# Kernel optimization log

Measured on AMD Instinct MI355X. Metric: run time of the kernel, lower is better.

The kernel has to match this reference:

```python
import jax, jax.numpy as jnp
import numpy as np

INPUT_SIZE = 512
UNITS = 1024


def setup_inputs() -> dict:
    key = jax.random.key(0)
    k_x, k_wih, k_whh, k_bih, k_bhh = jax.random.split(key, 5)
    B, T = 128, 512
    s_ih = 1.0 / np.sqrt(UNITS)
    return {
        "inputs": jax.random.normal(k_x, (B, T, INPUT_SIZE), dtype=jnp.float32),
        # torch nn.LSTMCell params: gate order i, f, g, o
        "W_ih": jax.random.uniform(k_wih, (4 * UNITS, INPUT_SIZE), minval=-s_ih, maxval=s_ih, dtype=jnp.float32),
        "W_hh": jax.random.uniform(k_whh, (4 * UNITS, UNITS), minval=-s_ih, maxval=s_ih, dtype=jnp.float32),
        "b_ih": jax.random.uniform(k_bih, (4 * UNITS,), minval=-s_ih, maxval=s_ih, dtype=jnp.float32),
        "b_hh": jax.random.uniform(k_bhh, (4 * UNITS,), minval=-s_ih, maxval=s_ih, dtype=jnp.float32),
    }


def reference(inputs, W_ih, W_hh, b_ih, b_hh):
    B, T, _ = inputs.shape
    U = W_hh.shape[1]
    # Precompute input contribution for all timesteps: [B, T, 4U]
    x_gates = jnp.einsum('bti,gi->btg', inputs, W_ih) + b_ih + b_hh

    def step(carry, xg):
        h, c = carry
        gates = xg + h @ W_hh.T  # [B, 4U]
        i, f, g, o = jnp.split(gates, 4, axis=-1)
        i = jax.nn.sigmoid(i)
        f = jax.nn.sigmoid(f)
        g = jnp.tanh(g)
        o = jax.nn.sigmoid(o)
        c = f * c + i * g
        h = o * jnp.tanh(c)
        return (h, c), h

    h0 = jnp.zeros((B, U), dtype=inputs.dtype)
    c0 = jnp.zeros((B, U), dtype=inputs.dtype)
    _, hs = jax.lax.scan(step, (h0, c0), jnp.swapaxes(x_gates, 0, 1))
    return jnp.swapaxes(hs, 0, 1)  # [B, T, U] (return_sequences=True)
```

## Files before the change

kernel.cpp:

```cpp
#include <hip/hip_runtime.h>
#include <hip/hip_bf16.h>

typedef __attribute__((ext_vector_type(8))) short short8;
typedef __attribute__((ext_vector_type(4))) float f32x4;
typedef unsigned int u32;
typedef unsigned short u16;

#define T_STEPS 512
#define B_SZ    128
#define I_SZ    512
#define U_SZ    1024
#define K_TOT   1536

#define XB_OFF   0
#define WC_OFF   67108864
#define FLAG_OFF 79691776
#define HBUF_OFF 79708160

__device__ __forceinline__ u16 f2bf(float f) {
  u32 u = __float_as_uint(f);
  u32 r = (u + 0x7fffu + ((u >> 16) & 1u)) >> 16;
  return (u16)r;
}
__device__ __forceinline__ float sigm(float x) { return 1.f / (1.f + __expf(-x)); }
__device__ __forceinline__ float tanh_s(float x) {
  float ax = fabsf(x);
  float e  = __expf(-2.f * ax);
  float t  = (1.f - e) / (1.f + e);
  return copysignf(t, x);
}

__global__ void k_convX(const float* __restrict__ X, u16* __restrict__ Xb) {
  u32 i = blockIdx.x * 256u + threadIdx.x;
  float4 v = reinterpret_cast<const float4*>(X)[i];
  uint2 o;
  o.x = (u32)f2bf(v.x) | ((u32)f2bf(v.y) << 16);
  o.y = (u32)f2bf(v.z) | ((u32)f2bf(v.w) << 16);
  reinterpret_cast<uint2*>(Xb)[i] = o;
}

__global__ void k_packW(const float* __restrict__ Wih, const float* __restrict__ Whh,
                        u16* __restrict__ Wc) {
  const int gcol = blockIdx.x;
  for (int k = threadIdx.x; k < K_TOT; k += 256) {
    float v = (k < I_SZ) ? Wih[(size_t)gcol * I_SZ + k]
                         : Whh[(size_t)gcol * U_SZ + (k - I_SZ)];
    Wc[(size_t)gcol * K_TOT + k] = f2bf(v);
  }
}

__global__ void k_zero(u32* __restrict__ hz, u32* __restrict__ flags) {
  u32 i = blockIdx.x * 256u + threadIdx.x;
  if (i < 131072u)      hz[i] = 0u;
  else if (i < 131328u) flags[i - 131072u] = 0u;
}

__device__ __forceinline__ short8 ld_h16(const u16* p) {
  short8 r;
  asm volatile("global_load_dwordx4 %0, %1, off sc0 sc1" : "=v"(r) : "v"(p));
  return r;
}
__device__ __forceinline__ void st_h(u16* p, u32 v) {
  asm volatile("global_store_short %0, %1, off sc0 sc1" :: "v"(p), "v"(v) : "memory");
}
__device__ __forceinline__ short8 ld_w16(const u16* p) {
  short8 r;
  asm volatile("global_load_dwordx4 %0, %1, off" : "=v"(r) : "v"(p));
  return r;
}

__global__ __launch_bounds__(512, 2)
void lstm_scan(const u16* __restrict__ Xb, const u16* __restrict__ Wc,
               const float* __restrict__ bih, const float* __restrict__ bhh,
               u16* __restrict__ hbuf, u32* __restrict__ flags,
               float* __restrict__ out) {
  __shared__ __align__(16) float gbuf[8][64][36];

  const int tid  = threadIdx.x;
  const int wg   = blockIdx.x;
  const int cl   = wg >> 6;
  const int wloc = wg & 63;
  const int rb   = cl * 32;
  const int u0   = wloc * 16;
  const int wid  = tid >> 6;
  const int lane = tid & 63;
  const int l15  = lane & 15;
  const int kg   = lane >> 4;
  const int kw   = wid;

  short8 Bf[6][4];
  #pragma unroll
  for (int ct = 0; ct < 4; ++ct) {
    const int gcol = ct * 1024 + u0 + l15;
    const u16* wrow = Wc + (size_t)gcol * K_TOT;
    #pragma unroll
    for (int i = 0; i < 6; ++i) {
      const int k = (i * 8 + kw) * 32 + kg * 8;
      Bf[i][ct] = ld_w16(wrow + k);
    }
  }
  asm volatile("s_waitcnt vmcnt(0)" ::: "memory");
  __builtin_amdgcn_sched_barrier(0);

  const int b_l = tid >> 4;
  const int uu  = tid & 15;
  const int ug  = u0 + uu;
  float bsum[4];
  #pragma unroll
  for (int g = 0; g < 4; ++g) bsum[g] = bih[g * 1024 + ug] + bhh[g * 1024 + ug];
  float c_state = 0.f;
  float* orow = out + (size_t)(rb + b_l) * (T_STEPS * U_SZ) + ug;
  const int hidx = (rb + b_l) * U_SZ + ug;
  u32* myflag = flags + (cl << 6) + wloc;
  u32* pollp  = flags + (cl << 6) + lane;

  const int r0 = rb + l15;
  const int r1 = r0 + 16;
  const u16* xrow0 = Xb + (size_t)r0 * (T_STEPS * I_SZ);
  const u16* xrow1 = Xb + (size_t)r1 * (T_STEPS * I_SZ);

  for (int t = 0; t < T_STEPS; ++t) {
    const u16* hsrc = hbuf + ((t & 1) ^ 1) * (B_SZ * U_SZ);
    u16*       hdst = hbuf + (t & 1) * (B_SZ * U_SZ);
    const u16* px0 = xrow0 + (size_t)t * I_SZ;
    const u16* px1 = xrow1 + (size_t)t * I_SZ;

    f32x4 acc[2][4];
    #pragma unroll
    for (int rt = 0; rt < 2; ++rt)
      #pragma unroll
      for (int ct = 0; ct < 4; ++ct)
        acc[rt][ct] = (f32x4){0.f, 0.f, 0.f, 0.f};

    #pragma unroll
    for (int i = 0; i < 2; ++i) {
      const int k = (i * 8 + kw) * 32 + kg * 8;
      const short8 a0 = *reinterpret_cast<const short8*>(px0 + k);
      const short8 a1 = *reinterpret_cast<const short8*>(px1 + k);
      #pragma unroll
      for (int ct = 0; ct < 4; ++ct) {
        acc[0][ct] = __builtin_amdgcn_mfma_f32_16x16x32_bf16(a0, Bf[i][ct], acc[0][ct], 0, 0, 0);
        acc[1][ct] = __builtin_amdgcn_mfma_f32_16x16x32_bf16(a1, Bf[i][ct], acc[1][ct], 0, 0, 0);
      }
    }

    for (;;) {
      const u32 v = __hip_atomic_load(pollp, __ATOMIC_RELAXED, __HIP_MEMORY_SCOPE_AGENT);
      if (__all((int)(v >= (u32)t))) break;
      __builtin_amdgcn_s_sleep(1);
    }

    short8 hA[4][2];
    #pragma unroll
    for (int ih = 0; ih < 4; ++ih) {
      const int ku = ((2 + ih) * 8 + kw) * 32 + kg * 8 - 512;
      hA[ih][0] = ld_h16(hsrc + (size_t)r0 * U_SZ + ku);
      hA[ih][1] = ld_h16(hsrc + (size_t)r1 * U_SZ + ku);
    }
    asm volatile("s_waitcnt vmcnt(0)" ::: "memory");
    __builtin_amdgcn_sched_barrier(0);
    #pragma unroll
    for (int ih = 0; ih < 4; ++ih)
      #pragma unroll
      for (int ct = 0; ct < 4; ++ct) {
        acc[0][ct] = __builtin_amdgcn_mfma_f32_16x16x32_bf16(hA[ih][0], Bf[2 + ih][ct], acc[0][ct], 0, 0, 0);
        acc[1][ct] = __builtin_amdgcn_mfma_f32_16x16x32_bf16(hA[ih][1], Bf[2 + ih][ct], acc[1][ct], 0, 0, 0);
      }

    #pragma unroll
    for (int rt = 0; rt < 2; ++rt)
      #pragma unroll
      for (int ct = 0; ct < 4; ++ct)
        *reinterpret_cast<float4*>(&gbuf[kw][ct * 16 + l15][rt * 16 + kg * 4]) =
            *reinterpret_cast<float4*>(&acc[rt][ct]);
    __syncthreads();

    float gs[4];
    #pragma unroll
    for (int g = 0; g < 4; ++g) {
      float s = bsum[g];
      #pragma unroll
      for (int k2 = 0; k2 < 8; ++k2) s += gbuf[k2][g * 16 + uu][b_l];
      gs[g] = s;
    }
    const float ig = sigm(gs[0]);
    const float fg = sigm(gs[1]);
    const float gg = tanh_s(gs[2]);
    const float og = sigm(gs[3]);
    c_state = fg * c_state + ig * gg;
    const float h = og * tanh_s(c_state);

    st_h(hdst + hidx, (u32)f2bf(h));
    asm volatile("s_waitcnt vmcnt(0)" ::: "memory");
    __syncthreads();
    if (tid == 0)
      __hip_atomic_store(myflag, (u32)(t + 1), __ATOMIC_RELAXED, __HIP_MEMORY_SCOPE_AGENT);

    orow[(size_t)t * U_SZ] = h;
  }
}

extern "C" void kernel_launch(void* const* d_in, const int* in_sizes, int n_in,
                              void* d_out, int out_size, void* d_ws, size_t ws_size,
                              hipStream_t stream) {
  const float* X   = (const float*)d_in[0];
  const float* Wih = (const float*)d_in[1];
  const float* Whh = (const float*)d_in[2];
  const float* bih = (const float*)d_in[3];
  const float* bhh = (const float*)d_in[4];
  float* out = (float*)d_out;
  char*  ws  = (char*)d_ws;

  u16* Xb    = (u16*)(ws + XB_OFF);
  u16* Wc    = (u16*)(ws + WC_OFF);
  u32* flags = (u32*)(ws + FLAG_OFF);
  u16* hbuf  = (u16*)(ws + HBUF_OFF);

  hipLaunchKernelGGL(k_convX, dim3(32768), dim3(256), 0, stream, X, Xb);
  hipLaunchKernelGGL(k_packW, dim3(4096), dim3(256), 0, stream, Wih, Whh, Wc);
  hipLaunchKernelGGL(k_zero,  dim3(513),  dim3(256), 0, stream, (u32*)hbuf, flags);

  void* args[] = {(void*)&Xb, (void*)&Wc, (void*)&bih, (void*)&bhh,
                  (void*)&hbuf, (void*)&flags, (void*)&out};
  hipLaunchCooperativeKernel((void*)lstm_scan, dim3(256), dim3(512), args, 0, stream);
}
```

Baseline: 2.584 ms.

## Prefetch next-step input projection before barrier and poll only needed producer flags

The x-part of the gate MFMA for step t+1 is now computed right after the h store, before the store-completion wait and barrier. The goal is to hide that input projection and its global loads under the store latency and the inter-workgroup synchronization instead of leaving them on the critical path. Each wave now also polls only the flags of the workgroups whose h columns it reads, not all 64 in the cluster, which relaxes the dependency wait. The cost is the accumulators staying live across the loop boundary, which may raise register pressure.

```diff
diff --git a/kernel.cpp b/kernel.cpp
--- a/kernel.cpp
+++ b/kernel.cpp
@@ -112,37 +112,37 @@
   float* orow = out + (size_t)(rb + b_l) * (T_STEPS * U_SZ) + ug;
   const int hidx = (rb + b_l) * U_SZ + ug;
   u32* myflag = flags + (cl << 6) + wloc;
-  u32* pollp  = flags + (cl << 6) + lane;
+
+  const int pidx = (kw << 1) + (((lane >> 1) & 3) << 4) + (lane & 1);
+  const u32* pollp = flags + (cl << 6) + pidx;
 
   const int r0 = rb + l15;
   const int r1 = r0 + 16;
   const u16* xrow0 = Xb + (size_t)r0 * (T_STEPS * I_SZ);
   const u16* xrow1 = Xb + (size_t)r1 * (T_STEPS * I_SZ);
 
+  f32x4 acc[2][4];
+  #pragma unroll
+  for (int rt = 0; rt < 2; ++rt)
+    #pragma unroll
+    for (int ct = 0; ct < 4; ++ct)
+      acc[rt][ct] = (f32x4){0.f, 0.f, 0.f, 0.f};
+
+  #pragma unroll
+  for (int i = 0; i < 2; ++i) {
+    const int k = (i * 8 + kw) * 32 + kg * 8;
+    const short8 a0 = *reinterpret_cast<const short8*>(xrow0 + k);
+    const short8 a1 = *reinterpret_cast<const short8*>(xrow1 + k);
+    #pragma unroll
+    for (int ct = 0; ct < 4; ++ct) {
+      acc[0][ct] = __builtin_amdgcn_mfma_f32_16x16x32_bf16(a0, Bf[i][ct], acc[0][ct], 0, 0, 0);
+      acc[1][ct] = __builtin_amdgcn_mfma_f32_16x16x32_bf16(a1, Bf[i][ct], acc[1][ct], 0, 0, 0);
+    }
+  }
+
   for (int t = 0; t < T_STEPS; ++t) {
     const u16* hsrc = hbuf + ((t & 1) ^ 1) * (B_SZ * U_SZ);
     u16*       hdst = hbuf + (t & 1) * (B_SZ * U_SZ);
-    const u16* px0 = xrow0 + (size_t)t * I_SZ;
-    const u16* px1 = xrow1 + (size_t)t * I_SZ;
-
-    f32x4 acc[2][4];
-    #pragma unroll
-    for (int rt = 0; rt < 2; ++rt)
-      #pragma unroll
-      for (int ct = 0; ct < 4; ++ct)
-        acc[rt][ct] = (f32x4){0.f, 0.f, 0.f, 0.f};
-
-    #pragma unroll
-    for (int i = 0; i < 2; ++i) {
-      const int k = (i * 8 + kw) * 32 + kg * 8;
-      const short8 a0 = *reinterpret_cast<const short8*>(px0 + k);
-      const short8 a1 = *reinterpret_cast<const short8*>(px1 + k);
-      #pragma unroll
-      for (int ct = 0; ct < 4; ++ct) {
-        acc[0][ct] = __builtin_amdgcn_mfma_f32_16x16x32_bf16(a0, Bf[i][ct], acc[0][ct], 0, 0, 0);
-        acc[1][ct] = __builtin_amdgcn_mfma_f32_16x16x32_bf16(a1, Bf[i][ct], acc[1][ct], 0, 0, 0);
-      }
-    }
 
     for (;;) {
       const u32 v = __hip_atomic_load(pollp, __ATOMIC_RELAXED, __HIP_MEMORY_SCOPE_AGENT);
@@ -191,6 +191,29 @@
     const float h = og * tanh_s(c_state);
 
     st_h(hdst + hidx, (u32)f2bf(h));
+
+    #pragma unroll
+    for (int rt = 0; rt < 2; ++rt)
+      #pragma unroll
+      for (int ct = 0; ct < 4; ++ct)
+        acc[rt][ct] = (f32x4){0.f, 0.f, 0.f, 0.f};
+    if (t + 1 < T_STEPS) {
+      const u16* qx0 = xrow0 + (size_t)(t + 1) * I_SZ;
+      const u16* qx1 = xrow1 + (size_t)(t + 1) * I_SZ;
+      #pragma unroll
+      for (int i = 0; i < 2; ++i) {
+        const int k = (i * 8 + kw) * 32 + kg * 8;
+        const short8 a0 = *reinterpret_cast<const short8*>(qx0 + k);
+        const short8 a1 = *reinterpret_cast<const short8*>(qx1 + k);
+        #pragma unroll
+        for (int ct = 0; ct < 4; ++ct) {
+          acc[0][ct] = __builtin_amdgcn_mfma_f32_16x16x32_bf16(a0, Bf[i][ct], acc[0][ct], 0, 0, 0);
+          acc[1][ct] = __builtin_amdgcn_mfma_f32_16x16x32_bf16(a1, Bf[i][ct], acc[1][ct], 0, 0, 0);
+        }
+      }
+    }
+    __builtin_amdgcn_sched_barrier(0);
+
     asm volatile("s_waitcnt vmcnt(0)" ::: "memory");
     __syncthreads();
     if (tid == 0)
```

New measurement: 2.989 ms. +15.7%, slower.

## Split each workgroup's batch rows into two interleaved independent recurrence streams

Applied to the files above, without the earlier changes.

Each workgroup now processes its 32 batch rows as two 16-row streams with separate flag arrays and LDS reduction buffers, alternating between them every timestep. The intent is to let one stream's dependency wait overlap with the other stream's progress across workgroups. In exchange it doubles the number of barrier and flag synchronisations per step, halves MFMA work per phase, and no longer computes the input projection before polling.

```diff
diff --git a/kernel.cpp b/kernel.cpp
--- a/kernel.cpp
+++ b/kernel.cpp
@@ -52,7 +52,7 @@
 __global__ void k_zero(u32* __restrict__ hz, u32* __restrict__ flags) {
   u32 i = blockIdx.x * 256u + threadIdx.x;
   if (i < 131072u)      hz[i] = 0u;
-  else if (i < 131328u) flags[i - 131072u] = 0u;
+  else                  flags[i - 131072u] = 0u;
 }
 
 __device__ __forceinline__ short8 ld_h16(const u16* p) {
@@ -74,7 +74,8 @@
                const float* __restrict__ bih, const float* __restrict__ bhh,
                u16* __restrict__ hbuf, u32* __restrict__ flags,
                float* __restrict__ out) {
-  __shared__ __align__(16) float gbuf[8][64][36];
+  __shared__ __align__(16) float gbufA[8][64][20];
+  __shared__ __align__(16) float gbufB[8][64][20];
 
   const int tid  = threadIdx.x;
   const int wg   = blockIdx.x;
@@ -102,101 +103,103 @@
   asm volatile("s_waitcnt vmcnt(0)" ::: "memory");
   __builtin_amdgcn_sched_barrier(0);
 
-  const int b_l = tid >> 4;
-  const int uu  = tid & 15;
-  const int ug  = u0 + uu;
+  const int row4 = tid >> 4;
+  const int uu   = tid & 15;
+  const int ug   = u0 + uu;
+  const int r16  = row4 & 15;
+  const int myStream = row4 >> 4;
   float bsum[4];
   #pragma unroll
   for (int g = 0; g < 4; ++g) bsum[g] = bih[g * 1024 + ug] + bhh[g * 1024 + ug];
   float c_state = 0.f;
-  float* orow = out + (size_t)(rb + b_l) * (T_STEPS * U_SZ) + ug;
-  const int hidx = (rb + b_l) * U_SZ + ug;
-  u32* myflag = flags + (cl << 6) + wloc;
-  u32* pollp  = flags + (cl << 6) + lane;
-
-  const int r0 = rb + l15;
-  const int r1 = r0 + 16;
-  const u16* xrow0 = Xb + (size_t)r0 * (T_STEPS * I_SZ);
-  const u16* xrow1 = Xb + (size_t)r1 * (T_STEPS * I_SZ);
-
-  for (int t = 0; t < T_STEPS; ++t) {
+  float* orow = out + (size_t)(rb + row4) * (T_STEPS * U_SZ) + ug;
+  const int hidx = (rb + row4) * U_SZ + ug;
+
+  const u16* xrowA = Xb + (size_t)(rb + l15)      * (T_STEPS * I_SZ);
+  const u16* xrowB = Xb + (size_t)(rb + 16 + l15) * (T_STEPS * I_SZ);
+  int hoffA[4], hoffB[4];
+  #pragma unroll
+  for (int ih = 0; ih < 4; ++ih) {
+    const int ku = ((2 + ih) * 8 + kw) * 32 + kg * 8 - 512;
+    hoffA[ih] = (rb + l15) * U_SZ + ku;
+    hoffB[ih] = (rb + 16 + l15) * U_SZ + ku;
+  }
+
+  u32* flA_my = flags +       (cl << 6) + wloc;
+  u32* flB_my = flags + 256 + (cl << 6) + wloc;
+  const u32* flA_po = flags +       (cl << 6) + lane;
+  const u32* flB_po = flags + 256 + (cl << 6) + lane;
+
+  auto body = [&](int t, const u16* xrowS, const int* hoffS,
+                  const u32* flag_poll, u32* flag_my,
+                  float (*gbufS)[64][20], int sId) {
+    for (;;) {
+      const u32 v = __hip_atomic_load(flag_poll, __ATOMIC_RELAXED, __HIP_MEMORY_SCOPE_AGENT);
+      if (__all((int)(v >= (u32)t))) break;
+      __builtin_amdgcn_s_sleep(1);
+    }
     const u16* hsrc = hbuf + ((t & 1) ^ 1) * (B_SZ * U_SZ);
     u16*       hdst = hbuf + (t & 1) * (B_SZ * U_SZ);
-    const u16* px0 = xrow0 + (size_t)t * I_SZ;
-    const u16* px1 = xrow1 + (size_t)t * I_SZ;
-
-    f32x4 acc[2][4];
-    #pragma unroll
-    for (int rt = 0; rt < 2; ++rt)
+
+    short8 hA[4];
+    #pragma unroll
+    for (int ih = 0; ih < 4; ++ih) hA[ih] = ld_h16(hsrc + hoffS[ih]);
+
+    f32x4 acc[4];
+    #pragma unroll
+    for (int ct = 0; ct < 4; ++ct) acc[ct] = (f32x4){0.f, 0.f, 0.f, 0.f};
+    const u16* px = xrowS + (size_t)t * I_SZ;
+    #pragma unroll
+    for (int i = 0; i < 2; ++i) {
+      const int k = (i * 8 + kw) * 32 + kg * 8;
+      const short8 a = *reinterpret_cast<const short8*>(px + k);
       #pragma unroll
       for (int ct = 0; ct < 4; ++ct)
-        acc[rt][ct] = (f32x4){0.f, 0.f, 0.f, 0.f};
-
-    #pragma unroll
-    for (int i = 0; i < 2; ++i) {
-      const int k = (i * 8 + kw) * 32 + kg * 8;
-      const short8 a0 = *reinterpret_cast<const short8*>(px0 + k);
-      const short8 a1 = *reinterpret_cast<const short8*>(px1 + k);
-      #pragma unroll
-      for (int ct = 0; ct < 4; ++ct) {
-        acc[0][ct] = __builtin_amdgcn_mfma_f32_16x16x32_bf16(a0, Bf[i][ct], acc[0][ct], 0, 0, 0);
-        acc[1][ct] = __builtin_amdgcn_mfma_f32_16x16x32_bf16(a1, Bf[i][ct], acc[1][ct], 0, 0, 0);
-      }
-    }
-
-    for (;;) {
-      const u32 v = __hip_atomic_load(pollp, __ATOMIC_RELAXED, __HIP_MEMORY_SCOPE_AGENT);
-      if (__all((int)(v >= (u32)t))) break;
-      __builtin_amdgcn_s_sleep(1);
-    }
-
-    short8 hA[4][2];
-    #pragma unroll
-    for (int ih = 0; ih < 4; ++ih) {
-      const int ku = ((2 + ih) * 8 + kw) * 32 + kg * 8 - 512;
-      hA[ih][0] = ld_h16(hsrc + (size_t)r0 * U_SZ + ku);
-      hA[ih][1] = ld_h16(hsrc + (size_t)r1 * U_SZ + ku);
-    }
+        acc[ct] = __builtin_amdgcn_mfma_f32_16x16x32_bf16(a, Bf[i][ct], acc[ct], 0, 0, 0);
+    }
+
     asm volatile("s_waitcnt vmcnt(0)" ::: "memory");
     __builtin_amdgcn_sched_barrier(0);
     #pragma unroll
     for (int ih = 0; ih < 4; ++ih)
       #pragma unroll
-      for (int ct = 0; ct < 4; ++ct) {
-        acc[0][ct] = __builtin_amdgcn_mfma_f32_16x16x32_bf16(hA[ih][0], Bf[2 + ih][ct], acc[0][ct], 0, 0, 0);
-        acc[1][ct] = __builtin_amdgcn_mfma_f32_16x16x32_bf16(hA[ih][1], Bf[2 + ih][ct], acc[1][ct], 0, 0, 0);
+      for (int ct = 0; ct < 4; ++ct)
+        acc[ct] = __builtin_amdgcn_mfma_f32_16x16x32_bf16(hA[ih], Bf[2 + ih][ct], acc[ct], 0, 0, 0);
+
+    #pragma unroll
+    for (int ct = 0; ct < 4; ++ct)
+      *reinterpret_cast<float4*>(&gbufS[kw][ct * 16 + l15][kg * 4]) =
+          *reinterpret_cast<float4*>(&acc[ct]);
+    __syncthreads();
+
+    if (myStream == sId) {
+      float gs[4];
+      #pragma unroll
+      for (int g = 0; g < 4; ++g) {
+        float s = bsum[g];
+        #pragma unroll
+        for (int k2 = 0; k2 < 8; ++k2) s += gbufS[k2][g * 16 + uu][r16];
+        gs[g] = s;
       }
-
-    #pragma unroll
-    for (int rt = 0; rt < 2; ++rt)
-      #pragma unroll
-      for (int ct = 0; ct < 4; ++ct)
-        *reinterpret_cast<float4*>(&gbuf[kw][ct * 16 + l15][rt * 16 + kg * 4]) =
-            *reinterpret_cast<float4*>(&acc[rt][ct]);
-    __syncthreads();
-
-    float gs[4];
-    #pragma unroll
-    for (int g = 0; g < 4; ++g) {
-      float s = bsum[g];
-      #pragma unroll
-      for (int k2 = 0; k2 < 8; ++k2) s += gbuf[k2][g * 16 + uu][b_l];
-      gs[g] = s;
-    }
-    const float ig = sigm(gs[0]);
-    const float fg = sigm(gs[1]);
-    const float gg = tanh_s(gs[2]);
-    const float og = sigm(gs[3]);
-    c_state = fg * c_state + ig * gg;
-    const float h = og * tanh_s(c_state);
-
-    st_h(hdst + hidx, (u32)f2bf(h));
+      const float ig = sigm(gs[0]);
+      const float fg = sigm(gs[1]);
+      const float gg = tanh_s(gs[2]);
+      const float og = sigm(gs[3]);
+      c_state = fg * c_state + ig * gg;
+      const float h = og * tanh_s(c_state);
+      st_h(hdst + hidx, (u32)f2bf(h));
+      orow[(size_t)t * U_SZ] = h;
+    }
+
     asm volatile("s_waitcnt vmcnt(0)" ::: "memory");
     __syncthreads();
     if (tid == 0)
-      __hip_atomic_store(myflag, (u32)(t + 1), __ATOMIC_RELAXED, __HIP_MEMORY_SCOPE_AGENT);
-
-    orow[(size_t)t * U_SZ] = h;
+      __hip_atomic_store(flag_my, (u32)(t + 1), __ATOMIC_RELAXED, __HIP_MEMORY_SCOPE_AGENT);
+  };
+
+  for (int t = 0; t < T_STEPS; ++t) {
+    body(t, xrowA, hoffA, flA_po, flA_my, gbufA, 0);
+    body(t, xrowB, hoffB, flB_po, flB_my, gbufB, 1);
   }
 }
 
@@ -218,7 +221,7 @@
 
   hipLaunchKernelGGL(k_convX, dim3(32768), dim3(256), 0, stream, X, Xb);
   hipLaunchKernelGGL(k_packW, dim3(4096), dim3(256), 0, stream, Wih, Whh, Wc);
-  hipLaunchKernelGGL(k_zero,  dim3(513),  dim3(256), 0, stream, (u32*)hbuf, flags);
+  hipLaunchKernelGGL(k_zero,  dim3(514),  dim3(256), 0, stream, (u32*)hbuf, flags);
 
   void* args[] = {(void*)&Xb, (void*)&Wc, (void*)&bih, (void*)&bhh,
                   (void*)&hbuf, (void*)&flags, (void*)&out};
```

Result: slower. 3.323 ms (+28.6%).
